# Kernel tuning notes

Hardware: AMD Instinct MI355X
Metric: run time of the kernel (lower is better)

Reference implementation:

```python
import jax, jax.numpy as jnp
import numpy as np

Z, N, K, W = 131072, 64, 64, 32


def setup_inputs() -> dict:
    key = jax.random.key(0)
    k1, k2, k3 = jax.random.split(key, 3)
    features = jax.random.normal(k1, (Z, N), dtype=jnp.float32)
    # dense realization of the CG-derived mixing tensor 'wkij'
    mixing_matrix = jax.random.normal(k2, (W, K, N, N), dtype=jnp.float32) * 0.05
    weight = jax.random.normal(k3, (W,), dtype=jnp.float32)
    return {"features": features, "mixing_matrix": mixing_matrix, "weight": weight}


def reference(features, mixing_matrix, weight):
    # torch: einsum('w,wkij,zi,zj->zk', weight, mixing_matrix, features, features)
    # Contract the small path axis w first -> [K, N, N] (cheap, tiny output),
    # then the bilinear square over z. einsum chooses a GEMM-style path; the
    # [Z, N, N] outer-product side is the memory-bound part.
    M = jnp.einsum('w,wkij->kij', weight, mixing_matrix)  # [K, N, N]
    out = jnp.einsum('kij,zi,zj->zk', M, features, features)  # [Z, K]
    return out
```

## Files before the change

kernel.cpp:

```cpp
#include <hip/hip_runtime.h>
#include <stdint.h>

typedef __attribute__((ext_vector_type(8))) short short8;
typedef __attribute__((ext_vector_type(4))) float f32x4;
typedef __attribute__((ext_vector_type(2))) float v2f;

#define NCHUNK 32
#define BROWS  136
#define XROWD  130

__device__ __forceinline__ unsigned short f2bf_rne(float f) {
  unsigned u = __builtin_bit_cast(unsigned, f);
  u += 0x7fffu + ((u >> 16) & 1u);
  return (unsigned short)(u >> 16);
}
__device__ __forceinline__ unsigned pack_bf2(float p0, float p1) {
  return __builtin_amdgcn_perm(__builtin_bit_cast(unsigned, p1),
                               __builtin_bit_cast(unsigned, p0), 0x07060302u);
}

__global__ __launch_bounds__(256) void prep_kernel(const float* __restrict__ mix,
                                                   const float* __restrict__ wgt,
                                                   unsigned short* __restrict__ Bp) {
  __shared__ float4 red[256];
  const int tid = threadIdx.x;
  const int ws  = tid >> 6;
  const int tt  = tid & 63;
  const int t4  = blockIdx.x * 64 + tt;
  const float4* m4 = (const float4*)mix;
  float ax = 0.f, ay = 0.f, az = 0.f, aw = 0.f;
#pragma unroll
  for (int wi = 0; wi < 8; ++wi) {
    const int w = ws * 8 + wi;
    const float s = wgt[w];
    const float4 v = m4[w * 65536 + t4];
    ax += s * v.x; ay += s * v.y; az += s * v.z; aw += s * v.w;
  }
  red[tid] = (float4){ax, ay, az, aw};
  __syncthreads();
  if (tid < 64) {
    const float4 a = red[tid], b = red[tid + 64], c = red[tid + 128], d = red[tid + 192];
    ushort4 r;
    r.x = f2bf_rne(a.x + b.x + c.x + d.x);
    r.y = f2bf_rne(a.y + b.y + c.y + d.y);
    r.z = f2bf_rne(a.z + b.z + c.z + d.z);
    r.w = f2bf_rne(a.w + b.w + c.w + d.w);
    ((ushort4*)Bp)[blockIdx.x * 64 + tid] = r;
  }
}

__global__ __launch_bounds__(256, 2) void gemm_kernel(const float* __restrict__ X,
                                                      const unsigned short* __restrict__ Bp,
                                                      float* __restrict__ out) {
  __shared__ unsigned short ldsB[2][64 * BROWS];
  __shared__ unsigned ldsX[64 * XROWD];

  const int tid  = threadIdx.x;
  const int lane = tid & 63;
  const int wv   = tid >> 6;
  const int m    = lane & 15;
  const int q    = lane >> 4;
  const int zblk = blockIdx.x * 256;

  {
    const float4* X4 = (const float4*)(X + (size_t)zblk * 64);
    const int rr = lane;
    const int ms = rr & 15;
    const int fd = (rr >> 4) & 1;
    const int ih = rr >> 5;
    const int zl = wv * 64 + fd * 32 + ms;
    const int zh = zl + 16;
    const int dcol = wv * 32 + ms * 2 + fd;
#pragma unroll
    for (int c4 = 0; c4 < 8; ++c4) {
      const float4 ve = X4[zl * 16 + ih * 8 + c4];
      const float4 vo = X4[zh * 16 + ih * 8 + c4];
      float ae[4], ao[4];
      *(float4*)ae = ve; *(float4*)ao = vo;
      const int i0 = ih * 32 + c4 * 4;
#pragma unroll
      for (int r = 0; r < 4; ++r) {
        const unsigned pk = (unsigned)f2bf_rne(ae[r]) | ((unsigned)f2bf_rne(ao[r]) << 16);
        ldsX[(i0 + r) * XROWD + dcol] = pk;
      }
    }
  }
  {
#pragma unroll
    for (int it = 0; it < 4; ++it) {
      const int lin = tid + it * 256;
      const int row = lin >> 4;
      const int cc  = lin & 15;
      const uint4 v = *(const uint4*)(Bp + row * 4096 + cc * 8);
      *(uint4*)(&ldsB[0][row * BROWS + cc * 8]) = v;
    }
  }

  v2f jv2[4][8];
  {
    const float4* X4g = (const float4*)X;
#pragma unroll
    for (int f = 0; f < 4; ++f) {
      const int zg = zblk + wv * 64 + f * 16 + m;
#pragma unroll
      for (int h = 0; h < 2; ++h) {
        const float4 a = X4g[zg * 16 + h * 8 + q * 2];
        const float4 b = X4g[zg * 16 + h * 8 + q * 2 + 1];
        jv2[f][h * 4 + 0] = v2f{a.x, a.y};
        jv2[f][h * 4 + 1] = v2f{a.z, a.w};
        jv2[f][h * 4 + 2] = v2f{b.x, b.y};
        jv2[f][h * 4 + 3] = v2f{b.z, b.w};
      }
    }
  }

  f32x4 acc[4][4];
#pragma unroll
  for (int f = 0; f < 4; ++f)
#pragma unroll
    for (int g = 0; g < 4; ++g) acc[f][g] = f32x4{0.f, 0.f, 0.f, 0.f};

  __syncthreads();

  for (int c = 0; c < NCHUNK; ++c) {
    uint4 pre[4];
    const int cn = (c + 1) & (NCHUNK - 1);
#pragma unroll
    for (int it = 0; it < 4; ++it) {
      const int lin = tid + it * 256;
      const int row = lin >> 4;
      const int cc  = lin & 15;
      pre[it] = *(const uint4*)(Bp + row * 4096 + cn * 128 + cc * 8);
    }

    const unsigned short* Bl = ldsB[c & 1];

#pragma unroll
    for (int il = 0; il < 2; ++il) {
      const int i = c * 2 + il;
      const uint2 sv = *(const uint2*)(ldsX + i * XROWD + wv * 32 + m * 2);
      float sf[4];
      sf[0] = __builtin_bit_cast(float, sv.x << 16);
      sf[1] = __builtin_bit_cast(float, sv.x & 0xffff0000u);
      sf[2] = __builtin_bit_cast(float, sv.y << 16);
      sf[3] = __builtin_bit_cast(float, sv.y & 0xffff0000u);
#pragma unroll
      for (int h = 0; h < 2; ++h) {
        const unsigned short* bb = Bl + m * BROWS + il * 64 + h * 32 + q * 8;
        const short8 b0 = *(const short8*)(bb);
        const short8 b1 = *(const short8*)(bb + 16 * BROWS);
        const short8 b2 = *(const short8*)(bb + 32 * BROWS);
        const short8 b3 = *(const short8*)(bb + 48 * BROWS);
#pragma unroll
        for (int f = 0; f < 4; ++f) {
          const v2f s2 = v2f{sf[f], sf[f]};
          union { unsigned u[4]; short8 v; } A;
#pragma unroll
          for (int e = 0; e < 4; ++e) {
            const v2f pr = s2 * jv2[f][h * 4 + e];
            A.u[e] = pack_bf2(pr[0], pr[1]);
          }
          acc[f][0] = __builtin_amdgcn_mfma_f32_16x16x32_bf16(A.v, b0, acc[f][0], 0, 0, 0);
          acc[f][1] = __builtin_amdgcn_mfma_f32_16x16x32_bf16(A.v, b1, acc[f][1], 0, 0, 0);
          acc[f][2] = __builtin_amdgcn_mfma_f32_16x16x32_bf16(A.v, b2, acc[f][2], 0, 0, 0);
          acc[f][3] = __builtin_amdgcn_mfma_f32_16x16x32_bf16(A.v, b3, acc[f][3], 0, 0, 0);
        }
      }
    }

    {
      unsigned short* dst = ldsB[(c + 1) & 1];
#pragma unroll
      for (int it = 0; it < 4; ++it) {
        const int lin = tid + it * 256;
        const int row = lin >> 4;
        const int cc  = lin & 15;
        *(uint4*)(&dst[row * BROWS + cc * 8]) = pre[it];
      }
    }
    __syncthreads();
  }

#pragma unroll
  for (int f = 0; f < 4; ++f) {
    const int zr = zblk + wv * 64 + f * 16 + q * 4;
#pragma unroll
    for (int g = 0; g < 4; ++g)
#pragma unroll
      for (int r = 0; r < 4; ++r)
        out[(size_t)(zr + r) * 64 + g * 16 + m] = acc[f][g][r];
  }
}

extern "C" void kernel_launch(void* const* d_in, const int* in_sizes, int n_in,
                              void* d_out, int out_size, void* d_ws, size_t ws_size,
                              hipStream_t stream) {
  const float* X   = (const float*)d_in[0];
  const float* mix = (const float*)d_in[1];
  const float* wgt = (const float*)d_in[2];
  float* out = (float*)d_out;
  unsigned short* Bp = (unsigned short*)d_ws;

  prep_kernel<<<1024, 256, 0, stream>>>(mix, wgt, Bp);
  gemm_kernel<<<512, 256, 0, stream>>>(X, Bp, out);
}
```

Before: 163.6 us.

## Read B fragments directly from global memory instead of double-buffered LDS

Removes the LDS double buffer for the bf16 mixing matrix B, along with its per-chunk prefetch, store and __syncthreads. Each wave now loads its MFMA B fragments straight from global memory, relying on L1/L2 caching since B is only 512 KB and shared by all blocks. This cuts LDS use and barriers, which could raise occupancy. In exchange, every wave issues redundant global loads, and the MFMA loop can stall on global load latency.

```diff
diff --git a/kernel.cpp b/kernel.cpp
--- a/kernel.cpp
+++ b/kernel.cpp
@@ -6,7 +6,6 @@
 typedef __attribute__((ext_vector_type(2))) float v2f;
 
 #define NCHUNK 32
-#define BROWS  136
 #define XROWD  130
 
 __device__ __forceinline__ unsigned short f2bf_rne(float f) {
@@ -52,7 +51,6 @@
 __global__ __launch_bounds__(256, 2) void gemm_kernel(const float* __restrict__ X,
                                                       const unsigned short* __restrict__ Bp,
                                                       float* __restrict__ out) {
-  __shared__ unsigned short ldsB[2][64 * BROWS];
   __shared__ unsigned ldsX[64 * XROWD];
 
   const int tid  = threadIdx.x;
@@ -64,10 +62,9 @@
 
   {
     const float4* X4 = (const float4*)(X + (size_t)zblk * 64);
-    const int rr = lane;
-    const int ms = rr & 15;
-    const int fd = (rr >> 4) & 1;
-    const int ih = rr >> 5;
+    const int ms = lane & 15;
+    const int fd = (lane >> 4) & 1;
+    const int ih = lane >> 5;
     const int zl = wv * 64 + fd * 32 + ms;
     const int zh = zl + 16;
     const int dcol = wv * 32 + ms * 2 + fd;
@@ -83,16 +80,6 @@
         const unsigned pk = (unsigned)f2bf_rne(ae[r]) | ((unsigned)f2bf_rne(ao[r]) << 16);
         ldsX[(i0 + r) * XROWD + dcol] = pk;
       }
-    }
-  }
-  {
-#pragma unroll
-    for (int it = 0; it < 4; ++it) {
-      const int lin = tid + it * 256;
-      const int row = lin >> 4;
-      const int cc  = lin & 15;
-      const uint4 v = *(const uint4*)(Bp + row * 4096 + cc * 8);
-      *(uint4*)(&ldsB[0][row * BROWS + cc * 8]) = v;
     }
   }
 
@@ -122,19 +109,9 @@
 
   __syncthreads();
 
+  const unsigned short* brow = Bp + m * 4096 + q * 8;
+
   for (int c = 0; c < NCHUNK; ++c) {
-    uint4 pre[4];
-    const int cn = (c + 1) & (NCHUNK - 1);
-#pragma unroll
-    for (int it = 0; it < 4; ++it) {
-      const int lin = tid + it * 256;
-      const int row = lin >> 4;
-      const int cc  = lin & 15;
-      pre[it] = *(const uint4*)(Bp + row * 4096 + cn * 128 + cc * 8);
-    }
-
-    const unsigned short* Bl = ldsB[c & 1];
-
 #pragma unroll
     for (int il = 0; il < 2; ++il) {
       const int i = c * 2 + il;
@@ -146,11 +123,11 @@
       sf[3] = __builtin_bit_cast(float, sv.y & 0xffff0000u);
 #pragma unroll
       for (int h = 0; h < 2; ++h) {
-        const unsigned short* bb = Bl + m * BROWS + il * 64 + h * 32 + q * 8;
-        const short8 b0 = *(const short8*)(bb);
-        const short8 b1 = *(const short8*)(bb + 16 * BROWS);
-        const short8 b2 = *(const short8*)(bb + 32 * BROWS);
-        const short8 b3 = *(const short8*)(bb + 48 * BROWS);
+        const int toff = c * 128 + il * 64 + h * 32;
+        const short8 b0 = *(const short8*)(brow + toff);
+        const short8 b1 = *(const short8*)(brow + toff + 65536);
+        const short8 b2 = *(const short8*)(brow + toff + 131072);
+        const short8 b3 = *(const short8*)(brow + toff + 196608);
 #pragma unroll
         for (int f = 0; f < 4; ++f) {
           const v2f s2 = v2f{sf[f], sf[f]};
@@ -167,18 +144,6 @@
         }
       }
     }
-
-    {
-      unsigned short* dst = ldsB[(c + 1) & 1];
-#pragma unroll
-      for (int it = 0; it < 4; ++it) {
-        const int lin = tid + it * 256;
-        const int row = lin >> 4;
-        const int cc  = lin & 15;
-        *(uint4*)(&dst[row * BROWS + cc * 8]) = pre[it];
-      }
-    }
-    __syncthreads();
   }
 
 #pragma unroll
```

After: 221.6 us. 1.35x slower.
